# Optimization experiments

Hardware: AMD Instinct MI355X
Metric: run time of the kernel (lower is better)

The kernel has to match this reference:

```python
import math
import jax, jax.numpy as jnp
import numpy as np

B, T, C = 2, 2048, 1024
H = 16
HD = C // H
WIN = 33
HALF = WIN // 2
CAUSAL = True
RADIUS, OMEGA, KSPR, STEP = 6.0, 1.0, 1.0, 0.1
EPS = 1e-8


def _spiral_step(x):
    # x: (..., 3) — the stacked (q, k, v) axis; D=3 -> rotate (x0, x1) pair.
    r = jnp.maximum(jnp.linalg.norm(x, axis=-1, keepdims=True), EPS)
    radial = (RADIUS - r) * (x / r)
    c = jnp.float32(math.cos(OMEGA * STEP))
    s = jnp.float32(math.sin(OMEGA * STEP))
    xi, xj, xl = x[..., 0], x[..., 1], x[..., 2]
    y = jnp.stack([c * xi - s * xj, s * xi + c * xj, xl], axis=-1)
    return x + STEP * (y - x + KSPR * radial)


def setup_inputs() -> dict:
    key = jax.random.key(0)
    ks = jax.random.split(key, 3)
    x = jax.random.normal(ks[0], (B, T, C), dtype=jnp.float32)
    W_attn = jax.random.normal(ks[1], (C, 3 * C), dtype=jnp.float32) * (1.0 / math.sqrt(C))
    W_proj = jax.random.normal(ks[2], (C, C), dtype=jnp.float32) * (1.0 / math.sqrt(C))
    sinks = jnp.zeros((H,), dtype=jnp.float32)
    ln_scale = jnp.ones((1,), dtype=jnp.float32) * 0.9
    ln_delta = jnp.ones((C,), dtype=jnp.float32)
    ln_bias = jnp.zeros((C,), dtype=jnp.float32)
    return {"x": x, "W_attn": W_attn, "W_proj": W_proj, "sinks": sinks,
            "ln_scale": ln_scale, "ln_delta": ln_delta, "ln_bias": ln_bias}


def reference(x, W_attn, W_proj, sinks, ln_scale, ln_delta, ln_bias):
    qkv = x @ W_attn                              # (B,T,3C)
    q, k, v = jnp.split(qkv, 3, axis=-1)          # each (B,T,C)

    # SpiralMix over the stacked (q,k,v) axis, loop_iters=2. Only q,k are
    # taken from the mixed output (v stays the pre-spiral value), matching src.
    s = jnp.stack([q, k, v], axis=-1)             # (B,T,C,3)
    s = _spiral_step(_spiral_step(s))
    q, k = s[..., 0], s[..., 1]

    def to_heads(t):
        return t.reshape(B, T, H, HD).transpose(0, 2, 1, 3)  # (B,H,T,hd)
    q, k, v = to_heads(q), to_heads(k), to_heads(v)

    # local window index
    t_idx = jnp.arange(T)
    offs = jnp.arange(-HALF, HALF + 1)
    neigh = t_idx[:, None] + offs[None, :]                    # (T,W)
    valid = (neigh >= 0) & (neigh < T)
    if CAUSAL:
        valid &= neigh <= t_idx[:, None]
    neigh_c = jnp.clip(neigh, 0, T - 1)

    k_n = k[:, :, neigh_c, :]                                 # (B,H,T,W,hd)
    v_n = v[:, :, neigh_c, :]

    inv_sqrt_d = 1.0 / math.sqrt(HD)
    scores = jnp.einsum('bhtd,bhtwd->bhtw',
                        q.astype(jnp.float32), k_n.astype(jnp.float32)) * inv_sqrt_d
    scores = jnp.where(valid[None, None], scores, -jnp.inf)

    # softmax with learned sink logits per head
    sinks_b = sinks.reshape(1, H, 1, 1).astype(scores.dtype)
    m = jnp.max(scores, axis=-1, keepdims=True)
    mj = jnp.maximum(m, sinks_b)
    exp_s = jnp.exp(scores - mj)
    denom = jnp.sum(exp_s, axis=-1, keepdims=True) + jnp.exp(sinks_b - mj)
    att = exp_s / denom                                       # (B,H,T,W)

    y = jnp.einsum('bhtw,bhtwd->bhtd', att, v_n.astype(att.dtype))
    y = y.transpose(0, 2, 1, 3).reshape(B, T, C).astype(x.dtype)
    y = y @ W_proj
    y = jnp.tanh(ln_scale * y)
    return ln_delta * y + ln_bias
```

## Files before the change

### kernel.cpp

```cpp
#include <hip/hip_runtime.h>
#include <hip/hip_fp16.h>
#include <math.h>

#define T_DIM 2048
#define B_DIM 2
#define C_DIM 1024
#define H_DIM 16
#define M_DIM 4096

typedef _Float16 f16x8 __attribute__((ext_vector_type(8)));
typedef _Float16 f16x4 __attribute__((ext_vector_type(4)));
typedef _Float16 f16x2 __attribute__((ext_vector_type(2)));
typedef float    f32x4 __attribute__((ext_vector_type(4)));

union f16x8_u { f16x8 v; f16x2 h[4]; _Float16 e[8]; };

#if defined(__has_builtin)
#  if __has_builtin(__builtin_amdgcn_fdot2)
#    define HAVE_FDOT2 1
#  endif
#endif

static __device__ __forceinline__ float FDOT2(f16x2 a, f16x2 b, float c)
{
#ifdef HAVE_FDOT2
    return __builtin_amdgcn_fdot2(a, b, c, false);
#else
    return c + (float)a[0] * (float)b[0] + (float)a[1] * (float)b[1];
#endif
}

#define ASYNC_COPY16(gsrc, ldst) \
  __builtin_amdgcn_global_load_lds( \
    (__attribute__((address_space(1))) unsigned int*)(gsrc), \
    (__attribute__((address_space(3))) unsigned int*)(ldst), 16, 0, 0)

__global__ __launch_bounds__(256) void conv_x_kernel(const float* __restrict__ x,
                                                     _Float16* __restrict__ xh, int n4)
{
    int i = blockIdx.x * 256 + threadIdx.x;
    if (i >= n4) return;
    float4 v = ((const float4*)x)[i];
    f16x4 o;
    o[0] = (_Float16)v.x; o[1] = (_Float16)v.y;
    o[2] = (_Float16)v.z; o[3] = (_Float16)v.w;
    ((f16x4*)xh)[i] = o;
}

__global__ __launch_bounds__(256) void transpose_f16_kernel(const float* __restrict__ W,
                                                            _Float16* __restrict__ WT,
                                                            int K, int N)
{
    __shared__ float tile[32][33];
    const int nbk = K >> 5;
    const int bk = blockIdx.x % nbk;
    const int bn = blockIdx.x / nbk;
    const int tx = threadIdx.x & 31, ty = threadIdx.x >> 5;
#pragma unroll
    for (int r = ty; r < 32; r += 8)
        tile[r][tx] = W[(long)(bk * 32 + r) * N + bn * 32 + tx];
    __syncthreads();
#pragma unroll
    for (int r = ty; r < 32; r += 8)
        WT[(long)(bn * 32 + r) * K + bk * 32 + tx] = (_Float16)tile[tx][r];
}

template<int BM, int EPI, int OUTF16>
__global__ __launch_bounds__(256) void gemm_f16_kernel(
    const _Float16* __restrict__ A, const _Float16* __restrict__ Bt,
    void* __restrict__ Cv, int M, int N, int K,
    const float* __restrict__ ln_scale, const float* __restrict__ ln_delta,
    const float* __restrict__ ln_bias)
{
    constexpr int M_REP   = BM / 32;
    constexpr int A_LOADS = BM / 64;
    __shared__ __attribute__((aligned(16))) _Float16 As[2][BM * 32];
    __shared__ __attribute__((aligned(16))) _Float16 Bs[2][128 * 32];

    const int tid  = threadIdx.x;
    const int lane = tid & 63;
    const int wave = tid >> 6;
    const int wr = wave >> 1, wc = wave & 1;
    const int ntn = N >> 7;
    const int m0 = (blockIdx.x / ntn) * BM;
    const int n0 = (blockIdx.x % ntn) << 7;

    f32x4 acc[M_REP][4] = {};

    const int ea = tid * 8;
    const _Float16* aptr[A_LOADS];
    const _Float16* bptr[2];
#pragma unroll
    for (int l = 0; l < A_LOADS; ++l) {
        const int e = ea + l * 2048;
        aptr[l] = A + (long)(m0 + (e >> 5)) * K + (e & 31);
    }
#pragma unroll
    for (int l = 0; l < 2; ++l) {
        const int e = ea + l * 2048;
        bptr[l] = Bt + (long)(n0 + (e >> 5)) * K + (e & 31);
    }

    const int fr = lane & 15;
    const int kb = (lane >> 4) << 3;
    const int NT = K >> 5;

#pragma unroll
    for (int l = 0; l < A_LOADS; ++l) ASYNC_COPY16(aptr[l], &As[0][ea + l * 2048]);
#pragma unroll
    for (int l = 0; l < 2; ++l)       ASYNC_COPY16(bptr[l], &Bs[0][ea + l * 2048]);
    asm volatile("s_waitcnt vmcnt(0)" ::: "memory");
    __syncthreads();

    int cur = 0;
    for (int t = 0; t < NT; ++t) {
        if (t + 1 < NT) {
            const int k0 = (t + 1) << 5;
#pragma unroll
            for (int l = 0; l < A_LOADS; ++l) ASYNC_COPY16(aptr[l] + k0, &As[cur ^ 1][ea + l * 2048]);
#pragma unroll
            for (int l = 0; l < 2; ++l)       ASYNC_COPY16(bptr[l] + k0, &Bs[cur ^ 1][ea + l * 2048]);
        }
        f16x8 af[M_REP], bf[4];
#pragma unroll
        for (int i = 0; i < M_REP; i++)
            af[i] = *(const f16x8*)&As[cur][((wr * (BM / 2) + (i << 4) + fr) << 5) + kb];
#pragma unroll
        for (int j = 0; j < 4; j++)
            bf[j] = *(const f16x8*)&Bs[cur][(((wc << 6) + (j << 4) + fr) << 5) + kb];
        __builtin_amdgcn_s_setprio(1);
#pragma unroll
        for (int i = 0; i < M_REP; i++)
#pragma unroll
            for (int j = 0; j < 4; j++)
                acc[i][j] = __builtin_amdgcn_mfma_f32_16x16x32_f16(af[i], bf[j], acc[i][j], 0, 0, 0);
        __builtin_amdgcn_s_setprio(0);
        if (t + 1 < NT) {
            asm volatile("s_waitcnt vmcnt(0)" ::: "memory");
            __syncthreads();
            cur ^= 1;
        }
    }

    const int rsub = (lane >> 4) << 2;
    const float lsc = EPI ? ln_scale[0] : 0.f;
#pragma unroll
    for (int j = 0; j < 4; j++) {
        const int col = n0 + (wc << 6) + (j << 4) + fr;
        float ld = 0.f, lb = 0.f;
        if (EPI) { ld = ln_delta[col]; lb = ln_bias[col]; }
#pragma unroll
        for (int i = 0; i < M_REP; i++) {
            const int rbase = m0 + wr * (BM / 2) + (i << 4) + rsub;
#pragma unroll
            for (int r = 0; r < 4; r++) {
                float v = acc[i][j][r];
                if (EPI) v = ld * tanhf(lsc * v) + lb;
                if (OUTF16) ((_Float16*)Cv)[(long)(rbase + r) * N + col] = (_Float16)v;
                else        ((float*)Cv)[(long)(rbase + r) * N + col] = v;
            }
        }
    }
}

__device__ __forceinline__ void spiral2(float& xi, float& xj, float xl)
{
    const float CS = 0.9950041652780258f;
    const float SN = 0.09983341664682815f;
#pragma unroll
    for (int s = 0; s < 2; s++) {
        float r = sqrtf(xi * xi + xj * xj + xl * xl);
        r = fmaxf(r, 1e-8f);
        const float coef = (6.0f - r) / r;
        const float yi = CS * xi - SN * xj;
        const float yj = SN * xi + CS * xj;
        const float nxi = xi + 0.1f * (yi - xi + coef * xi);
        const float nxj = xj + 0.1f * (yj - xj + coef * xj);
        const float nxl = xl + 0.1f * (coef * xl);
        xi = nxi; xj = nxj; xl = nxl;
    }
}

#define TB   128
#define ROWS 144
#define LDR  72

__global__ __launch_bounds__(128) void attn_kernel(const _Float16* __restrict__ qkv,
                                                   const float* __restrict__ sinks,
                                                   _Float16* __restrict__ yh)
{
    __shared__ __attribute__((aligned(16))) _Float16 k_lds[ROWS * LDR];
    __shared__ __attribute__((aligned(16))) _Float16 v_lds[ROWS * LDR];
    __shared__ __attribute__((aligned(16))) _Float16 q_lds[TB * LDR];

    const int tid = threadIdx.x;
    const int chunk = blockIdx.x & 15;
    const int h = (blockIdx.x >> 4) & 15;
    const int b = blockIdx.x >> 8;
    const int t0 = chunk * TB;
    const long bT = (long)b * T_DIM;

    for (int s = tid; s < ROWS * 4; s += 128) {
        const int ri = s >> 2, q4 = s & 3;
        const int gr = min(max(t0 - 16 + ri, 0), T_DIM - 1);
        const _Float16* base = qkv + (bT + gr) * 3072 + (h << 6) + (q4 << 4);
        f16x8_u qa, qb, ka, kb2, va, vb;
        qa.v  = *(const f16x8*)(base);        qb.v  = *(const f16x8*)(base + 8);
        ka.v  = *(const f16x8*)(base + 1024); kb2.v = *(const f16x8*)(base + 1032);
        va.v  = *(const f16x8*)(base + 2048); vb.v  = *(const f16x8*)(base + 2056);
        float qq[16], kk[16], vv[16];
#pragma unroll
        for (int u = 0; u < 8; u++) {
            qq[u] = (float)qa.e[u]; qq[8 + u] = (float)qb.e[u];
            kk[u] = (float)ka.e[u]; kk[8 + u] = (float)kb2.e[u];
            vv[u] = (float)va.e[u]; vv[8 + u] = (float)vb.e[u];
        }
#pragma unroll
        for (int u = 0; u < 16; u++) spiral2(qq[u], kk[u], vv[u]);
        const int lbase = ri * LDR + (q4 << 4);
        f16x8_u ko0, ko1, vo0, vo1;
#pragma unroll
        for (int u = 0; u < 8; u++) {
            ko0.e[u] = (_Float16)kk[u]; ko1.e[u] = (_Float16)kk[8 + u];
            vo0.e[u] = (_Float16)vv[u]; vo1.e[u] = (_Float16)vv[8 + u];
        }
        *(f16x8*)&k_lds[lbase]     = ko0.v;
        *(f16x8*)&k_lds[lbase + 8] = ko1.v;
        *(f16x8*)&v_lds[lbase]     = vo0.v;
        *(f16x8*)&v_lds[lbase + 8] = vo1.v;
        if (ri >= 16) {
            const int qbase = (ri - 16) * LDR + (q4 << 4);
            f16x8_u qo0, qo1;
#pragma unroll
            for (int u = 0; u < 8; u++) {
                qo0.e[u] = (_Float16)(qq[u] * 0.125f);
                qo1.e[u] = (_Float16)(qq[8 + u] * 0.125f);
            }
            *(f16x8*)&q_lds[qbase]     = qo0.v;
            *(f16x8*)&q_lds[qbase + 8] = qo1.v;
        }
    }
    __syncthreads();

    f16x8_u qv[8];
#pragma unroll
    for (int u = 0; u < 8; u++) qv[u].v = *(const f16x8*)&q_lds[tid * LDR + u * 8];

    float sc[17];
#pragma unroll
    for (int j = 0; j < 17; j++) {
        const _Float16* kr = &k_lds[(tid + j) * LDR];
        float s = 0.f;
#pragma unroll
        for (int u = 0; u < 8; u++) {
            f16x8_u kx; kx.v = *(const f16x8*)&kr[u * 8];
#pragma unroll
            for (int p = 0; p < 4; p++) s = FDOT2(qv[u].h[p], kx.h[p], s);
        }
        sc[j] = s;
    }

    const int t = t0 + tid;
#pragma unroll
    for (int j = 0; j < 17; j++)
        if (j + t < 16) sc[j] = -INFINITY;
    const float sink = sinks[h];
    float m = sink;
#pragma unroll
    for (int j = 0; j < 17; j++) m = fmaxf(m, sc[j]);
    float e[17];
    float denom = expf(sink - m);
#pragma unroll
    for (int j = 0; j < 17; j++) { e[j] = expf(sc[j] - m); denom += e[j]; }
    const float rden = 1.f / denom;
#pragma unroll
    for (int j = 0; j < 17; j++) e[j] *= rden;

    float yacc[64];
#pragma unroll
    for (int d = 0; d < 64; d++) yacc[d] = 0.f;
#pragma unroll
    for (int j = 0; j < 17; j++) {
        const float a = e[j];
        const _Float16* vr = &v_lds[(tid + j) * LDR];
#pragma unroll
        for (int u = 0; u < 8; u++) {
            f16x8_u vx; vx.v = *(const f16x8*)&vr[u * 8];
#pragma unroll
            for (int z = 0; z < 8; z++) yacc[u * 8 + z] += a * (float)vx.e[z];
        }
    }

#pragma unroll
    for (int u = 0; u < 8; u++) {
        f16x8_u yo;
#pragma unroll
        for (int z = 0; z < 8; z++) yo.e[z] = (_Float16)yacc[u * 8 + z];
        *(f16x8*)&q_lds[tid * LDR + u * 8] = yo.v;
    }
    __syncthreads();
    const int ch = tid & 7, rb = tid >> 3;
#pragma unroll
    for (int pass = 0; pass < 8; ++pass) {
        const int r = pass * 16 + rb;
        *(f16x8*)(yh + (bT + t0 + r) * 1024 + (h << 6) + ch * 8) =
            *(const f16x8*)&q_lds[r * LDR + ch * 8];
    }
}

extern "C" void kernel_launch(void* const* d_in, const int* in_sizes, int n_in,
                              void* d_out, int out_size, void* d_ws, size_t ws_size,
                              hipStream_t stream)
{
    const float* x        = (const float*)d_in[0];
    const float* W_attn   = (const float*)d_in[1];
    const float* W_proj   = (const float*)d_in[2];
    const float* sinks    = (const float*)d_in[3];
    const float* ln_scale = (const float*)d_in[4];
    const float* ln_delta = (const float*)d_in[5];
    const float* ln_bias  = (const float*)d_in[6];
    float* out = (float*)d_out;

    char* ws = (char*)d_ws;
    _Float16* xh    = (_Float16*)(ws);
    _Float16* WaT   = (_Float16*)(ws + (size_t)( 8u << 20));
    _Float16* WpT   = (_Float16*)(ws + (size_t)(14u << 20));
    _Float16* qkv16 = (_Float16*)(ws + (size_t)(16u << 20));
    _Float16* yh    = (_Float16*)(ws + (size_t)(40u << 20));

    conv_x_kernel<<<4096, 256, 0, stream>>>(x, xh, 1048576);
    transpose_f16_kernel<<<(1024 / 32) * (3072 / 32), 256, 0, stream>>>(W_attn, WaT, 1024, 3072);
    transpose_f16_kernel<<<(1024 / 32) * (1024 / 32), 256, 0, stream>>>(W_proj, WpT, 1024, 1024);
    gemm_f16_kernel<128, 0, 1><<<32 * 24, 256, 0, stream>>>(xh, WaT, qkv16, 4096, 3072, 1024,
                                                            nullptr, nullptr, nullptr);
    attn_kernel<<<512, 128, 0, stream>>>(qkv16, sinks, yh);
    gemm_f16_kernel<64, 1, 0><<<64 * 8, 256, 0, stream>>>(yh, WpT, out, 4096, 1024, 1024,
                                                          ln_scale, ln_delta, ln_bias);
}
```

Measured before the change: 182.6 us.

## Fuse prep kernels, triple-buffer GEMM loads, and swizzle workgroups across XCDs

The x conversion and both weight transposes are merged into one prep kernel launch, which removes two launches. The GEMM moves from double to triple buffering of its async global-to-LDS copies, so loads run two tiles ahead and partial vmcnt waits replace full drains. Workgroup IDs are remapped so consecutive tiles are spread across the 8 XCDs, which is meant to improve L2 reuse. In exchange the GEMM uses more LDS, and the hard-coded vmcnt counts depend on loads per thread.

```diff
diff --git a/kernel.cpp b/kernel.cpp
--- a/kernel.cpp
+++ b/kernel.cpp
@@ -35,27 +35,32 @@
     (__attribute__((address_space(1))) unsigned int*)(gsrc), \
     (__attribute__((address_space(3))) unsigned int*)(ldst), 16, 0, 0)
 
-__global__ __launch_bounds__(256) void conv_x_kernel(const float* __restrict__ x,
-                                                     _Float16* __restrict__ xh, int n4)
-{
-    int i = blockIdx.x * 256 + threadIdx.x;
-    if (i >= n4) return;
-    float4 v = ((const float4*)x)[i];
-    f16x4 o;
-    o[0] = (_Float16)v.x; o[1] = (_Float16)v.y;
-    o[2] = (_Float16)v.z; o[3] = (_Float16)v.w;
-    ((f16x4*)xh)[i] = o;
-}
-
-__global__ __launch_bounds__(256) void transpose_f16_kernel(const float* __restrict__ W,
-                                                            _Float16* __restrict__ WT,
-                                                            int K, int N)
+__global__ __launch_bounds__(256) void prep_kernel(const float* __restrict__ x,
+                                                   const float* __restrict__ Wa,
+                                                   const float* __restrict__ Wp,
+                                                   _Float16* __restrict__ xh,
+                                                   _Float16* __restrict__ WaT,
+                                                   _Float16* __restrict__ WpT)
 {
     __shared__ float tile[32][33];
-    const int nbk = K >> 5;
-    const int bk = blockIdx.x % nbk;
-    const int bn = blockIdx.x / nbk;
-    const int tx = threadIdx.x & 31, ty = threadIdx.x >> 5;
+    const int bid = blockIdx.x;
+    const int tid = threadIdx.x;
+    if (bid < 4096) {
+        const int i = bid * 256 + tid;
+        float4 v = ((const float4*)x)[i];
+        f16x4 o;
+        o[0] = (_Float16)v.x; o[1] = (_Float16)v.y;
+        o[2] = (_Float16)v.z; o[3] = (_Float16)v.w;
+        ((f16x4*)xh)[i] = o;
+        return;
+    }
+    const float* W; _Float16* WT; int N, b;
+    if (bid < 4096 + 3072) { W = Wa; WT = WaT; N = 3072; b = bid - 4096; }
+    else                   { W = Wp; WT = WpT; N = 1024; b = bid - 7168; }
+    const int K = 1024;
+    const int bk = b & 31;
+    const int bn = b >> 5;
+    const int tx = tid & 31, ty = tid >> 5;
 #pragma unroll
     for (int r = ty; r < 32; r += 8)
         tile[r][tx] = W[(long)(bk * 32 + r) * N + bn * 32 + tx];
@@ -74,16 +79,22 @@
 {
     constexpr int M_REP   = BM / 32;
     constexpr int A_LOADS = BM / 64;
-    __shared__ __attribute__((aligned(16))) _Float16 As[2][BM * 32];
-    __shared__ __attribute__((aligned(16))) _Float16 Bs[2][128 * 32];
+    constexpr int LPT     = A_LOADS + 2;
+    __shared__ __attribute__((aligned(16))) _Float16 As[3][BM * 32];
+    __shared__ __attribute__((aligned(16))) _Float16 Bs[3][128 * 32];
 
     const int tid  = threadIdx.x;
     const int lane = tid & 63;
     const int wave = tid >> 6;
     const int wr = wave >> 1, wc = wave & 1;
+
+    const int nwg = gridDim.x;
+    const int q8  = nwg >> 3;
+    const int bid = ((int)blockIdx.x & 7) * q8 + ((int)blockIdx.x >> 3);
+
     const int ntn = N >> 7;
-    const int m0 = (blockIdx.x / ntn) * BM;
-    const int n0 = (blockIdx.x % ntn) << 7;
+    const int m0 = (bid / ntn) * BM;
+    const int n0 = (bid % ntn) << 7;
 
     f32x4 acc[M_REP][4] = {};
 
@@ -105,29 +116,42 @@
     const int kb = (lane >> 4) << 3;
     const int NT = K >> 5;
 
-#pragma unroll
-    for (int l = 0; l < A_LOADS; ++l) ASYNC_COPY16(aptr[l], &As[0][ea + l * 2048]);
-#pragma unroll
-    for (int l = 0; l < 2; ++l)       ASYNC_COPY16(bptr[l], &Bs[0][ea + l * 2048]);
-    asm volatile("s_waitcnt vmcnt(0)" ::: "memory");
-    __syncthreads();
-
-    int cur = 0;
+    auto stage = [&](int tile, int slot) {
+        const int k0 = tile << 5;
+#pragma unroll
+        for (int l = 0; l < A_LOADS; ++l) ASYNC_COPY16(aptr[l] + k0, &As[slot][ea + l * 2048]);
+#pragma unroll
+        for (int l = 0; l < 2; ++l)       ASYNC_COPY16(bptr[l] + k0, &Bs[slot][ea + l * 2048]);
+    };
+
+    stage(0, 0);
+    stage(1, 1);
+
+    int s = 0;
     for (int t = 0; t < NT; ++t) {
-        if (t + 1 < NT) {
-            const int k0 = (t + 1) << 5;
-#pragma unroll
-            for (int l = 0; l < A_LOADS; ++l) ASYNC_COPY16(aptr[l] + k0, &As[cur ^ 1][ea + l * 2048]);
-#pragma unroll
-            for (int l = 0; l < 2; ++l)       ASYNC_COPY16(bptr[l] + k0, &Bs[cur ^ 1][ea + l * 2048]);
-        }
+        if (t + 2 < NT) {
+            int s2 = s + 2; if (s2 >= 3) s2 -= 3;
+            stage(t + 2, s2);
+        }
+        const int rem = NT - 1 - t;
+        if constexpr (LPT == 4) {
+            if (rem >= 2)      asm volatile("s_waitcnt vmcnt(8)" ::: "memory");
+            else if (rem == 1) asm volatile("s_waitcnt vmcnt(4)" ::: "memory");
+            else               asm volatile("s_waitcnt vmcnt(0)" ::: "memory");
+        } else {
+            if (rem >= 2)      asm volatile("s_waitcnt vmcnt(6)" ::: "memory");
+            else if (rem == 1) asm volatile("s_waitcnt vmcnt(3)" ::: "memory");
+            else               asm volatile("s_waitcnt vmcnt(0)" ::: "memory");
+        }
+        __syncthreads();
+
         f16x8 af[M_REP], bf[4];
 #pragma unroll
         for (int i = 0; i < M_REP; i++)
-            af[i] = *(const f16x8*)&As[cur][((wr * (BM / 2) + (i << 4) + fr) << 5) + kb];
+            af[i] = *(const f16x8*)&As[s][((wr * (BM / 2) + (i << 4) + fr) << 5) + kb];
 #pragma unroll
         for (int j = 0; j < 4; j++)
-            bf[j] = *(const f16x8*)&Bs[cur][(((wc << 6) + (j << 4) + fr) << 5) + kb];
+            bf[j] = *(const f16x8*)&Bs[s][(((wc << 6) + (j << 4) + fr) << 5) + kb];
         __builtin_amdgcn_s_setprio(1);
 #pragma unroll
         for (int i = 0; i < M_REP; i++)
@@ -135,11 +159,8 @@
             for (int j = 0; j < 4; j++)
                 acc[i][j] = __builtin_amdgcn_mfma_f32_16x16x32_f16(af[i], bf[j], acc[i][j], 0, 0, 0);
         __builtin_amdgcn_s_setprio(0);
-        if (t + 1 < NT) {
-            asm volatile("s_waitcnt vmcnt(0)" ::: "memory");
-            __syncthreads();
-            cur ^= 1;
-        }
+        if (t + 1 < NT) __syncthreads();
+        ++s; if (s == 3) s = 0;
     }
 
     const int rsub = (lane >> 4) << 2;
@@ -328,9 +349,7 @@
     _Float16* qkv16 = (_Float16*)(ws + (size_t)(16u << 20));
     _Float16* yh    = (_Float16*)(ws + (size_t)(40u << 20));
 
-    conv_x_kernel<<<4096, 256, 0, stream>>>(x, xh, 1048576);
-    transpose_f16_kernel<<<(1024 / 32) * (3072 / 32), 256, 0, stream>>>(W_attn, WaT, 1024, 3072);
-    transpose_f16_kernel<<<(1024 / 32) * (1024 / 32), 256, 0, stream>>>(W_proj, WpT, 1024, 1024);
+    prep_kernel<<<8192, 256, 0, stream>>>(x, W_attn, W_proj, xh, WaT, WpT);
     gemm_f16_kernel<128, 0, 1><<<32 * 24, 256, 0, stream>>>(xh, WaT, qkv16, 4096, 3072, 1024,
                                                             nullptr, nullptr, nullptr);
     attn_kernel<<<512, 128, 0, stream>>>(qkv16, sinks, yh);
```

New measurement: 173.2 us. 1.05x faster.
